# Optimization experiments

Hardware: AMD Instinct MI355X
Metric: run time of the kernel (lower is better)

The kernel has to match this reference:

```python
import jax, jax.numpy as jnp
import numpy as np

B, N, D = 4, 2048, 1024
H = 16
HD = D // H


def setup_inputs() -> dict:
    key = jax.random.key(0)
    ks = jax.random.split(key, 6)
    x = jax.random.normal(ks[0], (B, N, D), dtype=jnp.float32)
    # additive causal mask: 0 on/below diagonal, -inf above
    neg = jnp.float32(-1e9)
    causal_mask = jnp.where(jnp.triu(jnp.ones((N, N), dtype=bool), k=1), neg, 0.0).astype(jnp.float32)
    s = 1.0 / np.sqrt(D)
    Wqkv = jax.random.normal(ks[1], (D, 3 * D), dtype=jnp.float32) * s
    bqkv = jax.random.normal(ks[2], (3 * D,), dtype=jnp.float32) * 0.01
    Wproj = jax.random.normal(ks[3], (D, D), dtype=jnp.float32) * s
    bproj = jax.random.normal(ks[4], (D,), dtype=jnp.float32) * 0.01
    return {"x": x, "causal_mask": causal_mask, "Wqkv": Wqkv, "bqkv": bqkv, "Wproj": Wproj, "bproj": bproj}


def reference(x, causal_mask, Wqkv, bqkv, Wproj, bproj):
    b, n, d = x.shape
    qkv = x @ Wqkv + bqkv  # [B,N,3D]
    qkv = qkv.reshape(b, n, 3, H, HD).transpose(2, 0, 3, 1, 4)  # [3,B,H,N,HD]
    q, k, v = qkv[0], qkv[1], qkv[2]
    scale = HD ** -0.5
    attn = jnp.einsum('bhqd,bhkd->bhqk', q, k) * scale  # [B,H,N,N]
    attn = attn + causal_mask  # broadcast [N,N] -> [B,H,N,N]
    attn = jax.nn.softmax(attn, axis=-1)
    out = jnp.einsum('bhqk,bhkd->bhqd', attn, v)  # [B,H,N,HD]
    out = out.transpose(0, 2, 1, 3).reshape(b, n, d)
    return out @ Wproj + bproj
```

## Files before the change

### kernel.cpp

```cpp
#include <hip/hip_runtime.h>
#include <hip/hip_bf16.h>

typedef unsigned short u16;
typedef unsigned int u32;
typedef __attribute__((ext_vector_type(8))) short bf16x8;
typedef __attribute__((ext_vector_type(4))) float f32x4;
typedef __attribute__((ext_vector_type(16))) float f32x16;

#define AS1(p) ((const __attribute__((address_space(1))) void*)(p))
#define AS3(p) ((__attribute__((address_space(3))) void*)(p))
#define STG(src, dst) __builtin_amdgcn_global_load_lds(AS1(src), AS3(dst), 16, 0, 0)

#if __has_builtin(__builtin_amdgcn_exp2f)
#define EXP2F(x) __builtin_amdgcn_exp2f(x)
#else
#define EXP2F(x) exp2f(x)
#endif

static __device__ __forceinline__ float b2f(u16 u) {
  union { unsigned int i; float f; } v; v.i = ((unsigned int)u) << 16; return v.f;
}
static __device__ __forceinline__ u16 f2b(float f) {
  union { float f; unsigned int i; } v; v.f = f;
  unsigned int r = v.i + 0x7FFFu + ((v.i >> 16) & 1u);
  return (u16)(r >> 16);
}
static __device__ __forceinline__ u32 cvt_pk_bf16(float lo, float hi) {
  u32 r;
  asm("v_cvt_pk_bf16_f32 %0, %1, %2" : "=v"(r) : "v"(lo), "v"(hi));
  return r;
}
static __device__ __forceinline__ void permswap(u32& a, u32& b) {
  asm("v_permlane32_swap_b32 %0, %1" : "+v"(a), "+v"(b));
}

__global__ __launch_bounds__(256) void cast_f32_bf16(const float* __restrict__ src,
                                                     u16* __restrict__ dst, int n8) {
  int stride = gridDim.x * blockDim.x;
  for (int i = blockIdx.x * blockDim.x + threadIdx.x; i < n8; i += stride) {
    const float4* s = (const float4*)(src + (size_t)i * 8);
    float4 a = s[0], b = s[1];
    bf16x8 o;
    o[0] = (short)f2b(a.x); o[1] = (short)f2b(a.y); o[2] = (short)f2b(a.z); o[3] = (short)f2b(a.w);
    o[4] = (short)f2b(b.x); o[5] = (short)f2b(b.y); o[6] = (short)f2b(b.z); o[7] = (short)f2b(b.w);
    *(bf16x8*)(dst + (size_t)i * 8) = o;
  }
}

__global__ __launch_bounds__(256) void transpose_w(const float* __restrict__ src,
                                                   u16* __restrict__ dst,
                                                   int R, int C) {
  __shared__ float tile[32][33];
  int c0 = blockIdx.x * 32, r0 = blockIdx.y * 32;
  int tx = threadIdx.x, ty = threadIdx.y;
  for (int i = ty; i < 32; i += 8) tile[i][tx] = src[(size_t)(r0 + i) * C + c0 + tx];
  __syncthreads();
  for (int i = ty; i < 32; i += 8) dst[(size_t)(c0 + i) * R + r0 + tx] = f2b(tile[tx][i]);
}

__global__ __launch_bounds__(256) void transpose_v(const u16* __restrict__ qkv,
                                                   u16* __restrict__ VT) {
  const int N = 2048, TD = 3072, D = 1024;
  int bh = blockIdx.y, n0 = blockIdx.x * 64;
  int b = bh >> 4, h = bh & 15;
  int tid = threadIdx.x;
  __shared__ u16 tl[64][72];
  #pragma unroll
  for (int i = 0; i < 16; ++i) {
    int idx = tid + i * 256;
    int nl = idx >> 6, dd = idx & 63;
    tl[dd][nl] = qkv[(size_t)(b * N + n0 + nl) * TD + 2 * D + h * 64 + dd];
  }
  __syncthreads();
  #pragma unroll
  for (int i = 0; i < 16; ++i) {
    int idx = tid + i * 256;
    int dd = idx >> 6, nl = idx & 63;
    VT[((size_t)bh * 64 + dd) * N + n0 + nl] = tl[dd][nl];
  }
}

template <typename OutT>
__global__ __launch_bounds__(256, 2) void gemm256(
    const u16* __restrict__ A,
    const u16* __restrict__ BT,
    const float* __restrict__ bias,
    OutT* __restrict__ C,
    int M, int N, int K, int nn) {
  __shared__ alignas(16) u16 As[3][256 * 32];
  __shared__ alignas(16) u16 Bs[3][128 * 32];

  const int nwg = gridDim.x, cpx = nwg >> 3, id0 = blockIdx.x;
  const int swz = (id0 & 7) * cpx + (id0 >> 3);
  const int mi = swz / nn, ni = swz % nn;
  const int m0 = mi * 256, n0 = ni * 128;

  const int t = threadIdx.x;
  const int wid = t >> 6, lane = t & 63;
  const int wr = wid >> 1, wc = wid & 1;
  const int rlo = lane & 15, g = lane >> 4;

  const u16* aSrc[4];
  const u16* bSrc[2];
  int dA[4], dB[2];
  #pragma unroll
  for (int k = 0; k < 4; ++k) {
    const int c = t + 256 * k, cs = c ^ ((c >> 3) & 3);
    aSrc[k] = A + (size_t)(m0 + (cs >> 2)) * K + (cs & 3) * 8;
    dA[k] = c * 8;
  }
  #pragma unroll
  for (int k = 0; k < 2; ++k) {
    const int c = t + 256 * k, cs = c ^ ((c >> 3) & 3);
    bSrc[k] = BT + (size_t)(n0 + (cs >> 2)) * K + (cs & 3) * 8;
    dB[k] = c * 8;
  }

  f32x4 acc[8][4] = {};
  const int NT = K >> 5;

  #pragma unroll
  for (int k = 0; k < 4; ++k) STG(aSrc[k], &As[0][dA[k]]);
  #pragma unroll
  for (int k = 0; k < 2; ++k) STG(bSrc[k], &Bs[0][dB[k]]);
  #pragma unroll
  for (int k = 0; k < 4; ++k) STG(aSrc[k] + 32, &As[1][dA[k]]);
  #pragma unroll
  for (int k = 0; k < 2; ++k) STG(bSrc[k] + 32, &Bs[1][dB[k]]);

  int rb = 0, sb = 2;
  for (int kt = 0; kt < NT; ++kt) {
    __builtin_amdgcn_s_barrier();

    if (kt + 2 < NT) {
      const int ko = (kt + 2) * 32;
      #pragma unroll
      for (int k = 0; k < 4; ++k) STG(aSrc[k] + ko, &As[sb][dA[k]]);
      #pragma unroll
      for (int k = 0; k < 2; ++k) STG(bSrc[k] + ko, &Bs[sb][dB[k]]);
    }

    if (kt + 2 < NT)      asm volatile("s_waitcnt vmcnt(12)" ::: "memory");
    else if (kt + 1 < NT) asm volatile("s_waitcnt vmcnt(6)" ::: "memory");
    else                  asm volatile("s_waitcnt vmcnt(0)" ::: "memory");
    __builtin_amdgcn_s_barrier();

    const char* aB = (const char*)&As[rb][0];
    const char* bB = (const char*)&Bs[rb][0];
    bf16x8 a[8], b[4];
    #pragma unroll
    for (int fr = 0; fr < 8; ++fr) {
      const int r_ = wr * 128 + fr * 16 + rlo;
      a[fr] = *(const bf16x8*)(aB + (r_ * 64 + ((g ^ ((r_ >> 1) & 3)) << 4)));
    }
    #pragma unroll
    for (int fn = 0; fn < 4; ++fn) {
      const int r_ = wc * 64 + fn * 16 + rlo;
      b[fn] = *(const bf16x8*)(bB + (r_ * 64 + ((g ^ ((r_ >> 1) & 3)) << 4)));
    }
    __builtin_amdgcn_s_setprio(1);
    #pragma unroll
    for (int fr = 0; fr < 8; ++fr)
      #pragma unroll
      for (int fn = 0; fn < 4; ++fn)
        acc[fr][fn] = __builtin_amdgcn_mfma_f32_16x16x32_bf16(a[fr], b[fn], acc[fr][fn], 0, 0, 0);
    __builtin_amdgcn_s_setprio(0);

    rb = (rb == 2) ? 0 : rb + 1;
    sb = (sb == 2) ? 0 : sb + 1;
  }

  #pragma unroll
  for (int fn = 0; fn < 4; ++fn) {
    const int col = n0 + wc * 64 + fn * 16 + rlo;
    const float bv = bias[col];
    #pragma unroll
    for (int fr = 0; fr < 8; ++fr) {
      const int row = m0 + wr * 128 + fr * 16 + g * 4;
      #pragma unroll
      for (int i = 0; i < 4; ++i) {
        float r = acc[fr][fn][i] + bv;
        if constexpr (sizeof(OutT) == 2)
          C[(size_t)(row + i) * N + col] = (OutT)f2b(r);
        else
          C[(size_t)(row + i) * N + col] = (OutT)r;
      }
    }
  }
}

__global__ __launch_bounds__(256, 2) void attn_fwd(
    const u16* __restrict__ qkv,
    const u16* __restrict__ VT,
    u16* __restrict__ O) {
  const int N = 2048, TD = 3072, D = 1024;
  const int bid = blockIdx.x;
  const int qp = bid >> 6, bh = bid & 63;
  const int b = bh >> 4, h = bh & 15;
  const int t = threadIdx.x, w = t >> 6, lane = t & 63;
  const int l31 = lane & 31, hi = lane >> 5;
  const int qh = w >> 1, st = w & 1;

  __shared__ alignas(16) u16 pool16[2][64 * 64];
  __shared__ float rsLds[2][32];
  float* poolf = (float*)&pool16[0][0];

  const int c1 = t, c2 = t + 256;
  const int r1 = c1 >> 3, sc1 = ((c1 & 7) ^ (r1 & 7)) * 8;
  const int r2 = c2 >> 3, sc2 = ((c2 & 7) ^ (r2 & 7)) * 8;
  const u16* kbase = qkv + (size_t)(b * N) * TD + D + h * 64;
  const u16* vbase = VT + (size_t)bh * 64 * N;

  const float L2E = 1.44269504089f;
  const float NSH = -23.0830992f;

  for (int pass = 0; pass < 2; ++pass) {
    const int qt = pass ? (15 - qp) : qp;
    const int qbw = qt * 128 + qh * 64;

    bf16x8 qf[2][4];
    #pragma unroll
    for (int qs = 0; qs < 2; ++qs) {
      const u16* qp_ = qkv + ((size_t)(b * N) + qbw + qs * 32 + l31) * TD + h * 64 + hi * 8;
      #pragma unroll
      for (int c = 0; c < 4; ++c) {
        bf16x8 v = *(const bf16x8*)(qp_ + c * 16);
        #pragma unroll
        for (int j = 0; j < 8; ++j)
          v[j] = (short)f2b(b2f((u16)v[j]) * 0.125f);
        qf[qs][c] = v;
      }
    }

    f32x16 o_acc[2][2] = {};
    float psum[2] = {0.f, 0.f};
    const int jend = qt * 128 + 64;

    for (int j0 = 0; j0 <= jend; j0 += 64) {
      STG(kbase + (size_t)(j0 + r1) * TD + sc1, &pool16[0][c1 * 8]);
      STG(kbase + (size_t)(j0 + r2) * TD + sc2, &pool16[0][c2 * 8]);
      STG(vbase + (size_t)r1 * N + j0 + sc1, &pool16[1][c1 * 8]);
      STG(vbase + (size_t)r2 * N + j0 + sc2, &pool16[1][c2 * 8]);
      __syncthreads();

      const int sb2 = j0 + st * 32;
      if (sb2 <= qbw + 63) {
        bf16x8 kf[4];
        {
          const int row = st * 32 + l31, sw = (row & 7) << 3;
          #pragma unroll
          for (int c = 0; c < 4; ++c)
            kf[c] = *(const bf16x8*)&pool16[0][row * 64 + ((c * 16 + hi * 8) ^ sw)];
        }
        bf16x8 vf[2][2];
        #pragma unroll
        for (int dt = 0; dt < 2; ++dt) {
          const int row = dt * 32 + l31, sw = (row & 7) << 3;
          #pragma unroll
          for (int kc = 0; kc < 2; ++kc)
            vf[kc][dt] = *(const bf16x8*)&pool16[1][row * 64 + ((st * 32 + kc * 16 + hi * 8) ^ sw)];
        }

        #pragma unroll
        for (int qs = 0; qs < 2; ++qs) {
          if (qs == 0 && sb2 > qbw + 31) continue;
          const int qr = qbw + qs * 32 + l31;
          f32x16 S = {};
          __builtin_amdgcn_s_setprio(1);
          #pragma unroll
          for (int c = 0; c < 4; ++c)
            S = __builtin_amdgcn_mfma_f32_32x32x16_bf16(kf[c], qf[qs][c], S, 0, 0, 0);
          __builtin_amdgcn_s_setprio(0);
          if (sb2 + 31 > qbw + qs * 32) {
            const int kvb = sb2 + 4 * hi;
            #pragma unroll
            for (int r = 0; r < 16; ++r)
              if (kvb + (r & 3) + 8 * (r >> 2) > qr) S[r] = -1e30f;
          }
          float p[16];
          #pragma unroll
          for (int r = 0; r < 16; ++r) p[r] = EXP2F(fmaf(S[r], L2E, NSH));
          float ps = 0.f;
          #pragma unroll
          for (int r = 0; r < 16; ++r) ps += p[r];
          psum[qs] += ps;
          u32 wq[8];
          #pragma unroll
          for (int i = 0; i < 8; ++i) wq[i] = cvt_pk_bf16(p[2 * i], p[2 * i + 1]);
          permswap(wq[0], wq[2]); permswap(wq[1], wq[3]);
          permswap(wq[4], wq[6]); permswap(wq[5], wq[7]);
          union { u32 u[4]; bf16x8 v; } pa0, pa1;
          pa0.u[0] = wq[0]; pa0.u[1] = wq[1]; pa0.u[2] = wq[2]; pa0.u[3] = wq[3];
          pa1.u[0] = wq[4]; pa1.u[1] = wq[5]; pa1.u[2] = wq[6]; pa1.u[3] = wq[7];
          __builtin_amdgcn_s_setprio(1);
          #pragma unroll
          for (int dt = 0; dt < 2; ++dt) {
            o_acc[qs][dt] = __builtin_amdgcn_mfma_f32_32x32x16_bf16(pa0.v, vf[0][dt], o_acc[qs][dt], 0, 0, 0);
            o_acc[qs][dt] = __builtin_amdgcn_mfma_f32_32x32x16_bf16(pa1.v, vf[1][dt], o_acc[qs][dt], 0, 0, 0);
          }
          __builtin_amdgcn_s_setprio(0);
        }
      }
      __syncthreads();
    }

    float rsown[2];
    #pragma unroll
    for (int qs = 0; qs < 2; ++qs)
      rsown[qs] = psum[qs] + __shfl_xor(psum[qs], 32, 64);

    #pragma unroll
    for (int qs = 0; qs < 2; ++qs) {
      if (st != qs) {
        #pragma unroll
        for (int dt = 0; dt < 2; ++dt)
          #pragma unroll
          for (int r = 0; r < 16; ++r)
            poolf[qh * 2048 + (dt * 16 + r) * 64 + lane] = o_acc[qs][dt][r];
        rsLds[qh][l31] = rsown[qs];
      }
      __syncthreads();
      if (st == qs) {
        const float inv = 1.0f / (rsown[qs] + rsLds[qh][l31]);
        #pragma unroll
        for (int r = 0; r < 16; ++r) {
          const int qrow = (r & 3) + 8 * (r >> 2) + 4 * hi;
          const float invq = __shfl(inv, qrow, 64);
          const int q = qbw + qs * 32 + qrow;
          #pragma unroll
          for (int dt = 0; dt < 2; ++dt) {
            const float val = o_acc[qs][dt][r] + poolf[qh * 2048 + (dt * 16 + r) * 64 + lane];
            O[((size_t)(b * N) + q) * D + h * 64 + dt * 32 + l31] = f2b(val * invq);
          }
        }
      }
      __syncthreads();
    }
  }
}

extern "C" void kernel_launch(void* const* d_in, const int* in_sizes, int n_in,
                              void* d_out, int out_size, void* d_ws, size_t ws_size,
                              hipStream_t stream) {
  const float* x     = (const float*)d_in[0];
  const float* Wqkv  = (const float*)d_in[2];
  const float* bqkv  = (const float*)d_in[3];
  const float* Wproj = (const float*)d_in[4];
  const float* bproj = (const float*)d_in[5];
  float* out = (float*)d_out;

  const int B = 4, N = 2048, D = 1024, H = 16;
  const int BN = B * N;
  const int TD = 3 * D;

  char* ws = (char*)d_ws;
  u16* qkv    = (u16*)(ws);
  u16* vt     = (u16*)(ws + 50331648);
  u16* aout   = (u16*)(ws + 67108864);
  u16* wqkvT  = (u16*)(ws + 83886080);
  u16* wprojT = (u16*)(ws + 90177536);
  u16* xb     = (u16*)(ws + 92274688);

  cast_f32_bf16<<<2048, 256, 0, stream>>>(x, xb, BN * D / 8);
  transpose_w<<<dim3(TD / 32, D / 32), dim3(32, 8), 0, stream>>>(Wqkv, wqkvT, D, TD);
  transpose_w<<<dim3(D / 32, D / 32), dim3(32, 8), 0, stream>>>(Wproj, wprojT, D, D);
  gemm256<u16><<<768, 256, 0, stream>>>(xb, wqkvT, bqkv, qkv, BN, TD, D, 24);
  transpose_v<<<dim3(N / 64, B * H), 256, 0, stream>>>(qkv, vt);
  attn_fwd<<<512, 256, 0, stream>>>(qkv, vt, aout);
  gemm256<float><<<256, 256, 0, stream>>>(aout, wprojT, bproj, out, BN, D, D, 8);
}
```

Measured before the change: 195.5 us.

## Add 8-wave ping-pong 256x256 GEMM for QKV projection

Introduces a new GEMM kernel with 512 threads and 256x256 output tiles. It uses double-buffered LDS staged through global_load_lds, interleaves LDS fragment reads, async stages and MFMA quadrants between barriers, and raises MFMA priority with setprio. The QKV projection now uses this kernel in place of the 256x128 three-stage one, aiming for better operand reuse and load/compute overlap. The cost is one workgroup per CU and a complex barrier schedule that depends on K being a multiple of 128.

```diff
diff --git a/kernel.cpp b/kernel.cpp
--- a/kernel.cpp
+++ b/kernel.cpp
@@ -77,6 +77,129 @@
     int idx = tid + i * 256;
     int dd = idx >> 6, nl = idx & 63;
     VT[((size_t)bh * 64 + dd) * N + n0 + nl] = tl[dd][nl];
+  }
+}
+
+template <typename OutT>
+__global__ __launch_bounds__(512, 1) void gemm8p(
+    const u16* __restrict__ A,
+    const u16* __restrict__ BT,
+    const float* __restrict__ bias,
+    OutT* __restrict__ C,
+    int M, int N, int K, int nn) {
+  __shared__ alignas(16) u16 As[2][2][128 * 64];
+  __shared__ alignas(16) u16 Bs[2][2][128 * 64];
+
+  const int nwg = gridDim.x, cpx = nwg >> 3, id0 = blockIdx.x;
+  const int swz = (id0 & 7) * cpx + (id0 >> 3);
+  const int mi = swz / nn, ni = swz % nn;
+  const int m0 = mi * 256, n0 = ni * 256;
+
+  const int t = threadIdx.x;
+  const int wid = t >> 6, lane = t & 63;
+  const int wr = wid >> 2, wc = wid & 3;
+  const int rlo = lane & 15, g = lane >> 4;
+  const int swb = (rlo & 4) ? 32 : 0;
+
+  const int cs = t ^ (((t >> 5) & 1) << 1);
+  const int sr = cs >> 3, sc8 = (cs & 7) * 8;
+  const u16* aSH[2] = {A + (size_t)(m0 + sr) * K + sc8,
+                       A + (size_t)(m0 + 128 + sr) * K + sc8};
+  const u16* bSH[2] = {BT + (size_t)(n0 + sr) * K + sc8,
+                       BT + (size_t)(n0 + 128 + sr) * K + sc8};
+  const size_t rowK64 = (size_t)64 * K;
+
+  f32x4 acc[8][4] = {};
+  bf16x8 a[4][2], b[2][2];
+  const int NT = K >> 6;
+
+#define BAR() __builtin_amdgcn_s_barrier()
+#define VM2() asm volatile("s_waitcnt vmcnt(2)" ::: "memory")
+#define VM0() asm volatile("s_waitcnt vmcnt(0)" ::: "memory")
+#define STAGE_A(h, jt) do { if ((jt) < NT) { const size_t ko_ = (size_t)(jt) * 64; \
+    STG(aSH[h] + ko_, &As[(jt) & 1][h][t * 8]); \
+    STG(aSH[h] + ko_ + rowK64, &As[(jt) & 1][h][(t + 512) * 8]); } } while (0)
+#define STAGE_B(h, jt) do { if ((jt) < NT) { const size_t ko_ = (size_t)(jt) * 64; \
+    STG(bSH[h] + ko_, &Bs[(jt) & 1][h][t * 8]); \
+    STG(bSH[h] + ko_ + rowK64, &Bs[(jt) & 1][h][(t + 512) * 8]); } } while (0)
+#define RDA(buf, mh) _Pragma("unroll") for (int fr = 0; fr < 4; ++fr) \
+    _Pragma("unroll") for (int kc = 0; kc < 2; ++kc) { \
+      const int r_ = (mh) * 64 + fr * 16 + rlo; \
+      a[fr][kc] = *(const bf16x8*)((const char*)&As[buf][wr][0] + \
+                                   (((r_ * 64 + kc * 32 + g * 8) * 2) ^ swb)); }
+#define RDB(buf, nh) _Pragma("unroll") for (int fn = 0; fn < 2; ++fn) \
+    _Pragma("unroll") for (int kc = 0; kc < 2; ++kc) { \
+      const int r_ = (wc & 1) * 64 + (nh) * 32 + fn * 16 + rlo; \
+      b[fn][kc] = *(const bf16x8*)((const char*)&Bs[buf][wc >> 1][0] + \
+                                   (((r_ * 64 + kc * 32 + g * 8) * 2) ^ swb)); }
+#define MM(mh, nh) __builtin_amdgcn_s_setprio(1); \
+    _Pragma("unroll") for (int fr = 0; fr < 4; ++fr) \
+      _Pragma("unroll") for (int fn = 0; fn < 2; ++fn) { \
+        f32x4 v_ = acc[(mh) * 4 + fr][(nh) * 2 + fn]; \
+        v_ = __builtin_amdgcn_mfma_f32_16x16x32_bf16(a[fr][0], b[fn][0], v_, 0, 0, 0); \
+        v_ = __builtin_amdgcn_mfma_f32_16x16x32_bf16(a[fr][1], b[fn][1], v_, 0, 0, 0); \
+        acc[(mh) * 4 + fr][(nh) * 2 + fn] = v_; } \
+    __builtin_amdgcn_s_setprio(0)
+
+  STAGE_A(0, 0); STAGE_A(1, 0); STAGE_B(0, 0); STAGE_B(1, 0); STAGE_A(0, 1);
+  VM2(); BAR();
+
+  const int NI = NT >> 1;
+  #pragma unroll 1
+  for (int it = 0; it < NI; ++it) {
+    const int kt1 = 2 * it + 1;
+    RDA(0, 0) RDB(0, 0)
+    STAGE_A(1, kt1);
+    BAR(); MM(0, 0); BAR();
+    RDB(0, 1)
+    STAGE_B(0, kt1);
+    BAR(); MM(0, 1); BAR();
+    RDA(0, 1)
+    STAGE_B(1, kt1);
+    BAR(); MM(1, 1); BAR();
+    RDB(0, 0)
+    STAGE_A(0, kt1 + 1);
+    if (kt1 + 1 < NT) { VM2(); } else { VM0(); }
+    BAR(); MM(1, 0); BAR();
+    RDA(1, 0) RDB(1, 0)
+    STAGE_A(1, kt1 + 1);
+    BAR(); MM(0, 0); BAR();
+    RDB(1, 1)
+    STAGE_B(0, kt1 + 1);
+    BAR(); MM(0, 1); BAR();
+    RDA(1, 1)
+    STAGE_B(1, kt1 + 1);
+    BAR(); MM(1, 1); BAR();
+    RDB(1, 0)
+    STAGE_A(0, kt1 + 2);
+    if (kt1 + 1 < NT) { if (kt1 + 2 < NT) { VM2(); } else { VM0(); } }
+    BAR(); MM(1, 0); BAR();
+  }
+#undef BAR
+#undef VM2
+#undef VM0
+#undef STAGE_A
+#undef STAGE_B
+#undef RDA
+#undef RDB
+#undef MM
+
+  #pragma unroll
+  for (int nr = 0; nr < 4; ++nr) {
+    const int col = n0 + wc * 64 + nr * 16 + rlo;
+    const float bv = bias[col];
+    #pragma unroll
+    for (int mr = 0; mr < 8; ++mr) {
+      const int row = m0 + wr * 128 + mr * 16 + g * 4;
+      #pragma unroll
+      for (int i = 0; i < 4; ++i) {
+        float r = acc[mr][nr][i] + bv;
+        if constexpr (sizeof(OutT) == 2)
+          C[(size_t)(row + i) * N + col] = (OutT)f2b(r);
+        else
+          C[(size_t)(row + i) * N + col] = (OutT)r;
+      }
+    }
   }
 }
 
@@ -364,7 +487,7 @@
   cast_f32_bf16<<<2048, 256, 0, stream>>>(x, xb, BN * D / 8);
   transpose_w<<<dim3(TD / 32, D / 32), dim3(32, 8), 0, stream>>>(Wqkv, wqkvT, D, TD);
   transpose_w<<<dim3(D / 32, D / 32), dim3(32, 8), 0, stream>>>(Wproj, wprojT, D, D);
-  gemm256<u16><<<768, 256, 0, stream>>>(xb, wqkvT, bqkv, qkv, BN, TD, D, 24);
+  gemm8p<u16><<<384, 512, 0, stream>>>(xb, wqkvT, bqkv, qkv, BN, TD, D, 12);
   transpose_v<<<dim3(N / 64, B * H), 256, 0, stream>>>(qkv, vt);
   attn_fwd<<<512, 256, 0, stream>>>(qkv, vt, aout);
   gemm256<float><<<256, 256, 0, stream>>>(aout, wprojT, bproj, out, BN, D, D, 8);
```

Result: no change. 198.1 us (+1.3%).
